# Kernel tuning notes

Hardware: AMD Instinct MI355X
Metric: run time of the kernel (lower is better)

Reference implementation:

```python
import jax, jax.numpy as jnp
import numpy as np

P = 2        # patch size (all 3 dims)
NB = 8       # num_bands
N = 16       # d_state
DTR = 8      # dt_rank = d_model // 16
DCONV = 4    # d_conv
SMAX = 2.0   # smax_dt = smax_B = smax_C


def _ln(x, g, b):
    mu = x.mean(-1, keepdims=True)
    v = ((x - mu) ** 2).mean(-1, keepdims=True)
    return (x - mu) / jnp.sqrt(v + 1e-5) * g + b


def _silu(x):
    return x * jax.nn.sigmoid(x)


def _ssm_layer(x, band, m, rho, Win, bin_, convw, convb, Wx, Wdt, bdt, Alog, Dp,
               Wout, bout, edt, eB, eC, wr, wm):
    # x: [B, L, d_model] -> bidirectional conditioned selective scan (BiFCSSM)
    Bsz, L, _ = x.shape
    ED = convw.shape[0]
    xz = x @ Win + bin_
    xp, z = xz[..., :ED], xz[..., ED:]
    # depthwise causal conv1d over L
    xpad = jnp.pad(xp, ((0, 0), (DCONV - 1, 0), (0, 0)))
    xc = sum(xpad[:, k:k + L, :] * convw[:, k] for k in range(DCONV)) + convb
    xc = _silu(xc)
    dbl = xc @ Wx                                    # [B,L,DTR+2N]
    dt = jax.nn.softplus(dbl[..., :DTR] @ Wdt + bdt)  # [B,L,ED]
    # band/radius/mask conditioned modulation of delta, B, C
    s_dt = SMAX * jax.nn.sigmoid(edt[band][None] + wr[0] * rho[None] + wm[0] * m)
    s_B = SMAX * jax.nn.sigmoid(eB[band][None] + wr[1] * rho[None] + wm[1] * m)
    s_C = SMAX * jax.nn.sigmoid(eC[band][None] + wr[2] * rho[None] + wm[2] * m)
    dt = dt * s_dt[..., None]
    Bm = dbl[..., DTR:DTR + N] * s_B[..., None]       # [B,L,N]
    Cm = dbl[..., DTR + N:] * s_C[..., None]          # [B,L,N]
    A = -jnp.exp(Alog)                                # [ED,N]
    dA = jnp.exp(dt[..., None] * A)                   # [B,L,ED,N]
    dBu = (dA - 1.0) / A * Bm[:, :, None, :] * xc[..., None]   # exact ZOH
    dA_s = jnp.moveaxis(dA, 1, 0)
    dBu_s = jnp.moveaxis(dBu, 1, 0)
    C_s = jnp.moveaxis(Cm, 1, 0)
    h0 = jnp.zeros((Bsz, ED, N), x.dtype)

    def step(h, inp):
        a, bu, c = inp
        h = a * h + bu
        return h, jnp.einsum('ben,bn->be', h, c)

    _, yf = jax.lax.scan(step, h0, (dA_s, dBu_s, C_s))
    _, yb = jax.lax.scan(step, h0, (dA_s, dBu_s, C_s), reverse=True)
    y = jnp.moveaxis(yf + yb, 0, 1) + Dp * xc
    y = y * _silu(z)
    return y @ Wout + bout


def _fwd(kspace_ri, mask, pe_w, pe_b, pu_w, pu_b, ln_g, ln_b, fn_g, fn_b,
         cond_band, cond_rad_w, cond_mask_w, l0_Win, l0_bin, l0_convw, l0_convb,
         l0_Wx, l0_Wdt, l0_bdt, l0_Alog, l0_D, l0_Wout, l0_bout, l0_edt, l0_eB,
         l0_eC, l0_wr, l0_wm):
    Bsz, C, nx, ny, nz = kspace_ri.shape
    gx, gy, gz = nx // P, ny // P, nz // P
    L = gx * gy * gz
    # patch embed (Conv3d, kernel==stride) as blocked einsum
    xr = kspace_ri.reshape(Bsz, C, gx, P, gy, P, gz, P)
    x = jnp.einsum('bcxiyjzk,dcijk->bdxyz', xr, pe_w) + pe_b[None, :, None, None, None]
    DM = x.shape[1]
    x = x.reshape(Bsz, DM, L).transpose(0, 2, 1)               # [B,L,D]
    m = mask.reshape(Bsz, 1, gx, P, gy, P, gz, P).mean(axis=(3, 5, 7)).reshape(Bsz, L)
    m = jnp.clip(m, 0.0, 1.0)
    # raster scan ordering: identity permutation, rho_bar, band ids
    rho = jnp.arange(L, dtype=x.dtype) / float(L - 1)
    band = jnp.clip(jnp.floor(rho * NB).astype(jnp.int32), 0, NB - 1)
    # condition tokens
    cond = cond_band[band][None] + rho[None, :, None] * cond_rad_w + m[:, :, None] * cond_mask_w
    h = _ln(x + cond, ln_g, ln_b)
    h = h + _ssm_layer(_ln(h, fn_g, fn_b), band, m, rho, l0_Win, l0_bin, l0_convw,
                       l0_convb, l0_Wx, l0_Wdt, l0_bdt, l0_Alog, l0_D, l0_Wout,
                       l0_bout, l0_edt, l0_eB, l0_eC, l0_wr, l0_wm)
    # patch unembed (ConvTranspose3d, kernel==stride) as blocked einsum
    hg = h.transpose(0, 2, 1).reshape(Bsz, DM, gx, gy, gz)
    out = jnp.einsum('bdxyz,dcijk->bcxiyjzk', hg, pu_w).reshape(Bsz, C, nx, ny, nz)
    out = out + pu_b[None, :, None, None, None]
    return kspace_ri + out


def setup_inputs() -> dict:
    key = jax.random.key(0)
    ks = jax.random.split(key, 24)
    ED, DM, CIN = 256, 128, 16

    def nrm(k, shape, s):
        return jax.random.normal(k, shape, jnp.float32) * s

    return {
        'kspace_ri': jax.random.normal(ks[0], (1, CIN, 64, 64, 16), jnp.float32),
        'mask': jax.random.uniform(ks[1], (1, 1, 64, 64, 16), jnp.float32),
        'pe_w': nrm(ks[2], (DM, CIN, P, P, P), 0.09),
        'pe_b': nrm(ks[3], (DM,), 0.02),
        'pu_w': nrm(ks[4], (DM, CIN, P, P, P), 0.05),
        'pu_b': jnp.zeros((CIN,), jnp.float32),
        'ln_g': jnp.ones((DM,), jnp.float32),
        'ln_b': jnp.zeros((DM,), jnp.float32),
        'fn_g': jnp.ones((DM,), jnp.float32),
        'fn_b': jnp.zeros((DM,), jnp.float32),
        'cond_band': nrm(ks[5], (NB, DM), 0.02),
        'cond_rad_w': nrm(ks[6], (DM,), 0.02),
        'cond_mask_w': nrm(ks[7], (DM,), 0.02),
        'l0_Win': nrm(ks[8], (DM, 2 * ED), 0.05),
        'l0_bin': jnp.zeros((2 * ED,), jnp.float32),
        'l0_convw': nrm(ks[9], (ED, DCONV), 0.2),
        'l0_convb': jnp.zeros((ED,), jnp.float32),
        'l0_Wx': nrm(ks[10], (ED, DTR + 2 * N), 0.05),
        'l0_Wdt': nrm(ks[11], (DTR, ED), 0.1),
        'l0_bdt': jnp.full((ED,), -3.0, jnp.float32),
        'l0_Alog': jnp.log(jnp.tile(jnp.arange(1, N + 1, dtype=jnp.float32), (ED, 1))),
        'l0_D': jnp.ones((ED,), jnp.float32),
        'l0_Wout': nrm(ks[12], (ED, DM), 0.05),
        'l0_bout': jnp.zeros((DM,), jnp.float32),
        'l0_edt': nrm(ks[13], (NB,), 0.1),
        'l0_eB': nrm(ks[14], (NB,), 0.1),
        'l0_eC': nrm(ks[15], (NB,), 0.1),
        'l0_wr': nrm(ks[16], (3,), 0.1),
        'l0_wm': nrm(ks[17], (3,), 0.1),
    }


def reference(kspace_ri, mask, pe_w, pe_b, pu_w, pu_b, ln_g, ln_b, fn_g, fn_b,
              cond_band, cond_rad_w, cond_mask_w, l0_Win, l0_bin, l0_convw,
              l0_convb, l0_Wx, l0_Wdt, l0_bdt, l0_Alog, l0_D, l0_Wout, l0_bout,
              l0_edt, l0_eB, l0_eC, l0_wr, l0_wm):
    return _fwd(kspace_ri, mask, pe_w, pe_b, pu_w, pu_b, ln_g, ln_b, fn_g, fn_b,
                cond_band, cond_rad_w, cond_mask_w, l0_Win, l0_bin, l0_convw,
                l0_convb, l0_Wx, l0_Wdt, l0_bdt, l0_Alog, l0_D, l0_Wout, l0_bout,
                l0_edt, l0_eB, l0_eC, l0_wr, l0_wm)
```

## Files before the change

### kernel.cpp

```cpp
#include <hip/hip_runtime.h>
#include <hip/hip_bf16.h>

#define L_TOK 8192
#define NCh 512
#define CLh 16
#define NSEG 8
#define CPS (NCh / NSEG)
#define LOG2E 1.44269504088896f

typedef short bf16x8 __attribute__((ext_vector_type(8)));
typedef float f32x4 __attribute__((ext_vector_type(4)));

static __device__ __forceinline__ float nexp2(float x) {
#if __has_builtin(__builtin_amdgcn_exp2f)
    return __builtin_amdgcn_exp2f(x);
#else
    return exp2f(x);
#endif
}
static __device__ __forceinline__ float sigm(float x) {
    return 1.f / (1.f + nexp2(-x * LOG2E));
}
static __device__ __forceinline__ ushort f2bf(float x) {
    union { float f; uint u; } v; v.f = x;
    uint r = v.u + 0x7fffu + ((v.u >> 16) & 1u);
    return (ushort)(r >> 16);
}
static __device__ __forceinline__ float bf2f(ushort h) {
    union { float f; uint u; } v; v.u = ((uint)h) << 16;
    return v.f;
}
static __device__ __forceinline__ void f2hl(float x, ushort* hi, ushort* lo) {
    ushort h = f2bf(x);
    *hi = h;
    *lo = f2bf(x - bf2f(h));
}

#define W_PE   0
#define W_WIN  16384
#define W_WOUT 81920
#define W_PU   114688
#define W_PROJ 131072
#define W_TOT  212992

__global__ __launch_bounds__(256) void prep_k(const float* __restrict__ pe_w, const float* __restrict__ Win,
                                              const float* __restrict__ Wx, const float* __restrict__ Wdt,
                                              const float* __restrict__ Wout, const float* __restrict__ pu_w,
                                              const float* __restrict__ mask,
                                              ushort* __restrict__ wH, ushort* __restrict__ wL,
                                              float* __restrict__ mbuf) {
    int b = blockIdx.x;
    if (b >= 832) {
        int l = (b - 832) * 256 + threadIdx.x;
        int xg = l >> 8, yg = (l >> 3) & 31, zg = l & 7;
        float s = 0.f;
        for (int i2 = 0; i2 < 2; ++i2)
            for (int j2 = 0; j2 < 2; ++j2)
                for (int k2 = 0; k2 < 2; ++k2)
                    s += mask[(2 * xg + i2) * 1024 + (2 * yg + j2) * 16 + 2 * zg + k2];
        s *= 0.125f;
        mbuf[l] = fminf(fmaxf(s, 0.f), 1.f);
        return;
    }
    int i = b * 256 + threadIdx.x;
    float v;
    if (i < 16384) {
        v = pe_w[i];
    } else if (i < 81920) {
        int j = i - 16384; int n = j >> 7, k = j & 127;
        v = Win[k * 512 + n];
    } else if (i < 114688) {
        int j = i - 81920; int n = j >> 8, k = j & 255;
        v = Wout[k * 128 + n];
    } else if (i < 131072) {
        int j = i - 114688; int n = j >> 7, k = j & 127;
        v = pu_w[k * 128 + n];
    } else {
        int j = i - 131072; int n = j >> 8, k = j & 255;
        if (n < 256) {
            float s = 0.f;
#pragma unroll
            for (int r = 0; r < 8; ++r) s += Wx[k * 40 + r] * Wdt[r * 256 + n];
            v = s;
        } else if (n < 288) {
            v = Wx[k * 40 + 8 + (n - 256)];
        } else {
            v = 0.f;
        }
    }
    ushort h, lo; f2hl(v, &h, &lo);
    wH[i] = h; wL[i] = lo;
}

__global__ __launch_bounds__(256) void embed_ln_k(const float* __restrict__ ks,
                                                  const ushort* __restrict__ wH, const ushort* __restrict__ wL,
                                                  const float* __restrict__ pe_b, const float* __restrict__ cond_band,
                                                  const float* __restrict__ cond_rad, const float* __restrict__ cond_mask,
                                                  const float* __restrict__ mbuf,
                                                  const float* __restrict__ ln_g, const float* __restrict__ ln_b,
                                                  const float* __restrict__ fn_g, const float* __restrict__ fn_b,
                                                  float* __restrict__ h_,
                                                  ushort* __restrict__ hnH, ushort* __restrict__ hnL) {
    __shared__ __align__(16) char smem[50176];
    ushort (*AsH)[72] = (ushort(*)[72])(smem);
    ushort (*AsL)[72] = (ushort(*)[72])(smem + 2304);
    ushort (*BsH)[72] = (ushort(*)[72])(smem + 4608);
    ushort (*BsL)[72] = (ushort(*)[72])(smem + 23040);
    float*  ksb       = (float*)(smem + 41472);
    float  (*Cs)[132] = (float(*)[132])(smem);

    const int tid = threadIdx.x;
    const int lane = tid & 63, wn = tid >> 6;
    const int ln = lane & 15, q = lane >> 4;
    const int mb = blockIdx.x * 16;
    const int xg = mb >> 8, yg0 = (mb >> 3) & 31;

    for (int v = tid; v < 512; v += 256) {
        int seg = v >> 2, zq = v & 3;
        int cc = seg >> 3, i2 = (seg >> 2) & 1, yy = seg & 3;
        float4 t4 = *(const float4*)&ks[cc * 65536 + (2 * xg + i2) * 1024 + (2 * yg0 + yy) * 16 + zq * 4];
        int la = seg * 17 + zq * 4;
        ksb[la] = t4.x; ksb[la + 1] = t4.y; ksb[la + 2] = t4.z; ksb[la + 3] = t4.w;
    }

    f32x4 acc[2];
    acc[0] = (f32x4){0.f, 0.f, 0.f, 0.f};
    acc[1] = (f32x4){0.f, 0.f, 0.f, 0.f};

    for (int kc = 0; kc < 128; kc += 64) {
        __syncthreads();
        for (int u = tid; u < 1024; u += 256) {
            int r = u >> 6, kk = u & 63;
            int k = kc + kk;
            int cc = k >> 3, ijk = k & 7;
            int i2 = (ijk >> 2) & 1, j2 = (ijk >> 1) & 1, k2 = ijk & 1;
            int seg = (cc * 2 + i2) * 4 + (r >> 3) * 2 + j2;
            float v = ksb[seg * 17 + (r & 7) * 2 + k2];
            ushort hh, ll; f2hl(v, &hh, &ll);
            AsH[r][kk] = hh; AsL[r][kk] = ll;
        }
        for (int u = tid; u < 1024; u += 256) {
            int n = u >> 3, g = u & 7;
            *(uint4*)&BsH[n][g * 8] = *(const uint4*)&wH[W_PE + n * 128 + kc + g * 8];
            *(uint4*)&BsL[n][g * 8] = *(const uint4*)&wL[W_PE + n * 128 + kc + g * 8];
        }
        __syncthreads();
#pragma unroll
        for (int ks_ = 0; ks_ < 64; ks_ += 32) {
            const int kk = ks_ + q * 8;
            bf16x8 ah = *(const bf16x8*)&AsH[ln][kk];
            bf16x8 al = *(const bf16x8*)&AsL[ln][kk];
#pragma unroll
            for (int cb = 0; cb < 2; ++cb) {
                bf16x8 bh = *(const bf16x8*)&BsH[wn * 32 + cb * 16 + ln][kk];
                bf16x8 bl = *(const bf16x8*)&BsL[wn * 32 + cb * 16 + ln][kk];
                acc[cb] = __builtin_amdgcn_mfma_f32_16x16x32_bf16(ah, bh, acc[cb], 0, 0, 0);
                acc[cb] = __builtin_amdgcn_mfma_f32_16x16x32_bf16(ah, bl, acc[cb], 0, 0, 0);
                acc[cb] = __builtin_amdgcn_mfma_f32_16x16x32_bf16(al, bh, acc[cb], 0, 0, 0);
            }
        }
    }
    __syncthreads();
#pragma unroll
    for (int cb = 0; cb < 2; ++cb) {
#pragma unroll
        for (int r = 0; r < 4; ++r) {
            int row = q * 4 + r;
            int col = wn * 32 + cb * 16 + ln;
            int l = mb + row;
            float rho = (float)l * (1.0f / 8191.0f);
            int band = min(7, (int)(rho * 8.0f));
            Cs[row][col] = acc[cb][r] + pe_b[col] + cond_band[band * 128 + col]
                           + rho * cond_rad[col] + mbuf[l] * cond_mask[col];
        }
    }
    __syncthreads();
    {
        int row = tid >> 4, j = tid & 15;
        int l = mb + row;
        float v8[8];
        float s = 0.f, s2 = 0.f;
#pragma unroll
        for (int i = 0; i < 8; ++i) {
            float v = Cs[row][j * 8 + i];
            v8[i] = v; s += v; s2 += v * v;
        }
#pragma unroll
        for (int o = 1; o < 16; o <<= 1) { s += __shfl_xor(s, o, 16); s2 += __shfl_xor(s2, o, 16); }
        float mu = s * (1.f / 128.f);
        float var = s2 * (1.f / 128.f) - mu * mu;
        float rstd = rsqrtf(fmaxf(var, 0.f) + 1e-5f);
        float hv[8];
        s = 0.f; s2 = 0.f;
#pragma unroll
        for (int i = 0; i < 8; ++i) {
            int col = j * 8 + i;
            float h = (v8[i] - mu) * rstd * ln_g[col] + ln_b[col];
            hv[i] = h; s += h; s2 += h * h;
        }
#pragma unroll
        for (int i = 0; i < 8; i += 4)
            *(float4*)&h_[(size_t)l * 128 + j * 8 + i] = make_float4(hv[i], hv[i + 1], hv[i + 2], hv[i + 3]);
#pragma unroll
        for (int o = 1; o < 16; o <<= 1) { s += __shfl_xor(s, o, 16); s2 += __shfl_xor(s2, o, 16); }
        mu = s * (1.f / 128.f);
        var = s2 * (1.f / 128.f) - mu * mu;
        rstd = rsqrtf(fmaxf(var, 0.f) + 1e-5f);
        union { ushort u[8]; uint4 v4; } oh, ol;
#pragma unroll
        for (int i = 0; i < 8; ++i) {
            int col = j * 8 + i;
            float o2 = (hv[i] - mu) * rstd * fn_g[col] + fn_b[col];
            ushort hh, ll; f2hl(o2, &hh, &ll);
            oh.u[i] = hh; ol.u[i] = ll;
        }
        *(uint4*)&hnH[(size_t)l * 128 + j * 8] = oh.v4;
        *(uint4*)&hnL[(size_t)l * 128 + j * 8] = ol.v4;
    }
}

__global__ __launch_bounds__(256) void win_k(const ushort* __restrict__ Ah, const ushort* __restrict__ Al,
                                             const ushort* __restrict__ wH, const ushort* __restrict__ wL,
                                             const float* __restrict__ bin_,
                                             float* __restrict__ xp, float* __restrict__ sz) {
    __shared__ ushort AsH[64][72], AsL[64][72];
    __shared__ ushort BsH[64][72], BsL[64][72];
    const int tid = threadIdx.x;
    const int lane = tid & 63, wave = tid >> 6;
    const int wm = wave & 1, wn = wave >> 1;
    const int ln = lane & 15, q = lane >> 4;
    const int mb = blockIdx.x * 64, nb = blockIdx.y * 64;

    f32x4 acc[2][2];
#pragma unroll
    for (int rb = 0; rb < 2; ++rb)
#pragma unroll
        for (int cb = 0; cb < 2; ++cb) acc[rb][cb] = (f32x4){0.f, 0.f, 0.f, 0.f};

    for (int kc = 0; kc < 128; kc += 64) {
        __syncthreads();
        for (int u = tid; u < 512; u += 256) {
            int r = u >> 3, g = u & 7;
            size_t go = (size_t)(mb + r) * 128 + kc + g * 8;
            *(uint4*)&AsH[r][g * 8] = *(const uint4*)&Ah[go];
            *(uint4*)&AsL[r][g * 8] = *(const uint4*)&Al[go];
        }
        for (int u = tid; u < 512; u += 256) {
            int n = u >> 3, g = u & 7;
            size_t go = (size_t)(W_WIN) + (size_t)(nb + n) * 128 + kc + g * 8;
            *(uint4*)&BsH[n][g * 8] = *(const uint4*)&wH[go];
            *(uint4*)&BsL[n][g * 8] = *(const uint4*)&wL[go];
        }
        __syncthreads();
#pragma unroll
        for (int ks_ = 0; ks_ < 64; ks_ += 32) {
            const int kk = ks_ + q * 8;
            bf16x8 ah[2], al[2], bh[2], bl[2];
#pragma unroll
            for (int rb = 0; rb < 2; ++rb) {
                ah[rb] = *(const bf16x8*)&AsH[wm * 32 + rb * 16 + ln][kk];
                al[rb] = *(const bf16x8*)&AsL[wm * 32 + rb * 16 + ln][kk];
            }
#pragma unroll
            for (int cb = 0; cb < 2; ++cb) {
                bh[cb] = *(const bf16x8*)&BsH[wn * 32 + cb * 16 + ln][kk];
                bl[cb] = *(const bf16x8*)&BsL[wn * 32 + cb * 16 + ln][kk];
            }
#pragma unroll
            for (int rb = 0; rb < 2; ++rb)
#pragma unroll
                for (int cb = 0; cb < 2; ++cb) {
                    acc[rb][cb] = __builtin_amdgcn_mfma_f32_16x16x32_bf16(ah[rb], bh[cb], acc[rb][cb], 0, 0, 0);
                    acc[rb][cb] = __builtin_amdgcn_mfma_f32_16x16x32_bf16(ah[rb], bl[cb], acc[rb][cb], 0, 0, 0);
                    acc[rb][cb] = __builtin_amdgcn_mfma_f32_16x16x32_bf16(al[rb], bh[cb], acc[rb][cb], 0, 0, 0);
                }
        }
    }
#pragma unroll
    for (int rb = 0; rb < 2; ++rb)
#pragma unroll
        for (int cb = 0; cb < 2; ++cb)
#pragma unroll
            for (int r = 0; r < 4; ++r) {
                int l = mb + wm * 32 + rb * 16 + q * 4 + r;
                int col = nb + wn * 32 + cb * 16 + ln;
                float v = acc[rb][cb][r] + bin_[col];
                if (col < 256) {
                    xp[(size_t)l * 256 + col] = v;
                } else {
                    sz[(size_t)l * 256 + (col - 256)] = v * sigm(v);
                }
            }
}

__global__ __launch_bounds__(512) void proj_k(const float* __restrict__ xp,
                                              const float* __restrict__ convw, const float* __restrict__ convb,
                                              const ushort* __restrict__ wH, const ushort* __restrict__ wL,
                                              const float* __restrict__ bdt, const float* __restrict__ mbuf,
                                              const float* __restrict__ edt, const float* __restrict__ eB,
                                              const float* __restrict__ eC, const float* __restrict__ wr,
                                              const float* __restrict__ wm,
                                              float* __restrict__ xc, float* __restrict__ dt,
                                              float* __restrict__ Bm, float* __restrict__ Cm) {
    __shared__ __align__(16) char smem[52224];
    ushort (*AsH)[264] = (ushort(*)[264])(smem);
    ushort (*AsL)[264] = (ushort(*)[264])(smem + 16896);
    ushort (*BsH)[72]  = (ushort(*)[72])(smem + 33792);
    ushort (*BsL)[72]  = (ushort(*)[72])(smem + 43008);
    const int tid = threadIdx.x;
    const int mb = blockIdx.x * 32;

    {
        const int cg = tid & 63;
        const int rg = tid >> 6;
        const int c0 = cg * 4;
        float4 cb4 = *(const float4*)&convb[c0];
        float4 cw0 = *(const float4*)&convw[(c0 + 0) * 4];
        float4 cw1 = *(const float4*)&convw[(c0 + 1) * 4];
        float4 cw2 = *(const float4*)&convw[(c0 + 2) * 4];
        float4 cw3 = *(const float4*)&convw[(c0 + 3) * 4];
        const int lbase = mb + rg * 4;
        float4 zero = make_float4(0.f, 0.f, 0.f, 0.f);
        float4 x0 = (lbase - 3 >= 0) ? *(const float4*)&xp[(size_t)(lbase - 3) * 256 + c0] : zero;
        float4 x1 = (lbase - 2 >= 0) ? *(const float4*)&xp[(size_t)(lbase - 2) * 256 + c0] : zero;
        float4 x2 = (lbase - 1 >= 0) ? *(const float4*)&xp[(size_t)(lbase - 1) * 256 + c0] : zero;
#pragma unroll
        for (int rr = 0; rr < 4; ++rr) {
            int l = lbase + rr;
            float4 x3 = *(const float4*)&xp[(size_t)l * 256 + c0];
            float o0 = cb4.x + x0.x * cw0.x + x1.x * cw0.y + x2.x * cw0.z + x3.x * cw0.w;
            float o1 = cb4.y + x0.y * cw1.x + x1.y * cw1.y + x2.y * cw1.z + x3.y * cw1.w;
            float o2 = cb4.z + x0.z * cw2.x + x1.z * cw2.y + x2.z * cw2.z + x3.z * cw2.w;
            float o3 = cb4.w + x0.w * cw3.x + x1.w * cw3.y + x2.w * cw3.z + x3.w * cw3.w;
            o0 *= sigm(o0); o1 *= sigm(o1); o2 *= sigm(o2); o3 *= sigm(o3);
            *(float4*)&xc[(size_t)l * 256 + c0] = make_float4(o0, o1, o2, o3);
            union { ushort u[4]; uint2 v2; } hh, ll;
            f2hl(o0, &hh.u[0], &ll.u[0]); f2hl(o1, &hh.u[1], &ll.u[1]);
            f2hl(o2, &hh.u[2], &ll.u[2]); f2hl(o3, &hh.u[3], &ll.u[3]);
            int row = l - mb;
            *(uint2*)&AsH[row][c0] = hh.v2;
            *(uint2*)&AsL[row][c0] = ll.v2;
            x0 = x1; x1 = x2; x2 = x3;
        }
    }
    __syncthreads();

    const int lane = tid & 63, wave = tid >> 6;
    const int wm2 = wave & 1, wn4 = wave >> 1;
    const int ln = lane & 15, q = lane >> 4;
    for (int it = 0; it < 5; ++it) {
        int nb = it * 64;
        f32x4 acc = (f32x4){0.f, 0.f, 0.f, 0.f};
        for (int kc = 0; kc < 256; kc += 64) {
            __syncthreads();
            {
                int u = tid;
                int n = u >> 3, g = u & 7;
                size_t go = (size_t)(W_PROJ) + (size_t)(nb + n) * 256 + kc + g * 8;
                *(uint4*)&BsH[n][g * 8] = *(const uint4*)&wH[go];
                *(uint4*)&BsL[n][g * 8] = *(const uint4*)&wL[go];
            }
            __syncthreads();
#pragma unroll
            for (int ks_ = 0; ks_ < 64; ks_ += 32) {
                const int kka = kc + ks_ + q * 8;
                const int kkb = ks_ + q * 8;
                bf16x8 ah = *(const bf16x8*)&AsH[wm2 * 16 + ln][kka];
                bf16x8 al = *(const bf16x8*)&AsL[wm2 * 16 + ln][kka];
                bf16x8 bh = *(const bf16x8*)&BsH[wn4 * 16 + ln][kkb];
                bf16x8 bl = *(const bf16x8*)&BsL[wn4 * 16 + ln][kkb];
                acc = __builtin_amdgcn_mfma_f32_16x16x32_bf16(ah, bh, acc, 0, 0, 0);
                acc = __builtin_amdgcn_mfma_f32_16x16x32_bf16(ah, bl, acc, 0, 0, 0);
                acc = __builtin_amdgcn_mfma_f32_16x16x32_bf16(al, bh, acc, 0, 0, 0);
            }
        }
#pragma unroll
        for (int r = 0; r < 4; ++r) {
            int l = mb + wm2 * 16 + q * 4 + r;
            int col = nb + wn4 * 16 + ln;
            float v = acc[r];
            float rho = (float)l * (1.0f / 8191.0f);
            int band = min(7, (int)(rho * 8.0f));
            float mv = mbuf[l];
            if (col < 256) {
                float sc0 = 2.0f * sigm(edt[band] + wr[0] * rho + wm[0] * mv);
                float v2 = v + bdt[col];
                float sp = (v2 > 20.f) ? v2 : log1pf(expf(v2));
                dt[(size_t)l * 256 + col] = sp * sc0;
            } else if (col < 272) {
                float sc1 = 2.0f * sigm(eB[band] + wr[1] * rho + wm[1] * mv);
                Bm[(size_t)l * 16 + (col - 256)] = v * sc1;
            } else if (col < 288) {
                float sc2 = 2.0f * sigm(eC[band] + wr[2] * rho + wm[2] * mv);
                Cm[(size_t)l * 16 + (col - 272)] = v * sc2;
            }
        }
    }
}

__global__ __launch_bounds__(256, 4) void scan0_k(const float* __restrict__ dt, const float* __restrict__ xc,
                                                  const float* __restrict__ Bm, const float* __restrict__ Alog,
                                                  float* __restrict__ Hb, float* __restrict__ sdtb) {
    const int c = blockIdx.x, dir = blockIdx.y, e = threadIdx.x;
    __shared__ float bms[CLh][16];
    for (int idx = e; idx < CLh * 16; idx += 256)
        bms[idx >> 4][idx & 15] = Bm[c * (CLh * 16) + idx];
    float A2[16], iv[16], h[16];
#pragma unroll
    for (int n = 0; n < 16; ++n) {
        float ea = nexp2(Alog[e * 16 + n] * LOG2E);
        A2[n] = -ea * LOG2E;
        iv[n] = -1.0f / ea;
        h[n] = 0.f;
    }
    const int base = c * CLh;
    float cu[8], cx[8], nu[8], nx[8];
#pragma unroll
    for (int j = 0; j < 8; ++j) {
        int p = dir ? (CLh - 1 - j) : j;
        cu[j] = dt[(size_t)(base + p) * 256 + e];
        cx[j] = xc[(size_t)(base + p) * 256 + e];
    }
    __syncthreads();
    float sdt = 0.f;
#pragma unroll
    for (int g = 0; g < CLh / 8; ++g) {
        if (g + 1 < CLh / 8) {
#pragma unroll
            for (int j = 0; j < 8; ++j) {
                int s = (g + 1) * 8 + j;
                int p = dir ? (CLh - 1 - s) : s;
                nu[j] = dt[(size_t)(base + p) * 256 + e];
                nx[j] = xc[(size_t)(base + p) * 256 + e];
            }
        }
#pragma unroll
        for (int j = 0; j < 8; ++j) {
            int s = g * 8 + j;
            int p = dir ? (CLh - 1 - s) : s;
            float u = cu[j], xv = cx[j];
            union { float4 v[4]; float f[16]; } bb;
            const float4* bp = (const float4*)&bms[p][0];
            bb.v[0] = bp[0]; bb.v[1] = bp[1]; bb.v[2] = bp[2]; bb.v[3] = bp[3];
#pragma unroll
            for (int n = 0; n < 16; ++n) {
                float a = nexp2(A2[n] * u);
                float w = xv * bb.f[n] * iv[n];
                h[n] = a * (h[n] + w) - w;
            }
            sdt += u;
        }
#pragma unroll
        for (int j = 0; j < 8; ++j) { cu[j] = nu[j]; cx[j] = nx[j]; }
    }
    const size_t hofs = (size_t)(dir * NCh + c) * 4096 + e * 16;
#pragma unroll
    for (int j = 0; j < 4; ++j)
        *(float4*)&Hb[hofs + 4 * j] = make_float4(h[4 * j], h[4 * j + 1], h[4 * j + 2], h[4 * j + 3]);
    if (dir == 0) sdtb[c * 256 + e] = sdt;
}

__global__ __launch_bounds__(256) void combine1_k(const float* __restrict__ Hb, const float* __restrict__ sdtb,
                                                  const float* __restrict__ Alog,
                                                  float* __restrict__ Hpp, float* __restrict__ cumsdtb,
                                                  float* __restrict__ segq, float* __restrict__ segsdt) {
    const int gid = blockIdx.x * 256 + threadIdx.x;
    const int seg = gid >> 13;
    const int r = gid & 8191;
    const int d1 = r >> 12, en = r & 4095, e1 = en >> 4;
    const float A2e = -nexp2(Alog[en] * LOG2E) * LOG2E;
    float hi = 0.f, cum = 0.f;
    for (int k = 0; k < CPS; ++k) {
        const int pos = seg * CPS + k;
        const int c2 = d1 ? (NCh - 1 - pos) : pos;
        const size_t o2 = (size_t)(d1 * NCh + c2) * 4096 + en;
        const float sv = sdtb[c2 * 256 + e1];
        Hpp[o2] = hi;
        if ((en & 15) == 0) cumsdtb[(d1 * NCh + c2) * 256 + e1] = cum;
        hi = nexp2(A2e * sv) * hi + Hb[o2];
        cum += sv;
    }
    segq[(d1 * NSEG + seg) * 4096 + en] = hi;
    if ((en & 15) == 0) segsdt[(d1 * NSEG + seg) * 256 + e1] = cum;
}

__global__ __launch_bounds__(64) void combine2_k(const float* __restrict__ segq, const float* __restrict__ segsdt,
                                                 const float* __restrict__ Alog, float* __restrict__ segpre) {
    const int gid = blockIdx.x * 64 + threadIdx.x;
    const int d1 = gid >> 12, en = gid & 4095, e1 = en >> 4;
    const float A2e = -nexp2(Alog[en] * LOG2E) * LOG2E;
    float hi = 0.f;
#pragma unroll
    for (int s = 0; s < NSEG; ++s) {
        segpre[(d1 * NSEG + s) * 4096 + en] = hi;
        hi = nexp2(A2e * segsdt[(d1 * NSEG + s) * 256 + e1]) * hi + segq[(d1 * NSEG + s) * 4096 + en];
    }
}

template <int DIR>
static __device__ __forceinline__ void scan_dir(const float* __restrict__ dt, const float* __restrict__ xc,
                                                int base, int e,
                                                const float (*bms)[16], const float (*cms)[16],
                                                const float* A2, const float* iv,
                                                float* h, float* yreg) {
    float cu[8], cx[8], nu[8], nx[8];
#pragma unroll
    for (int j = 0; j < 8; ++j) {
        const int p = DIR ? (CLh - 1 - j) : j;
        cu[j] = dt[(size_t)(base + p) * 256 + e];
        cx[j] = xc[(size_t)(base + p) * 256 + e];
    }
#pragma unroll
    for (int g = 0; g < CLh / 8; ++g) {
        if (g + 1 < CLh / 8) {
#pragma unroll
            for (int j = 0; j < 8; ++j) {
                const int s = (g + 1) * 8 + j;
                const int p = DIR ? (CLh - 1 - s) : s;
                nu[j] = dt[(size_t)(base + p) * 256 + e];
                nx[j] = xc[(size_t)(base + p) * 256 + e];
            }
        }
#pragma unroll
        for (int j = 0; j < 8; ++j) {
            const int s = g * 8 + j;
            const int p = DIR ? (CLh - 1 - s) : s;
            float u = cu[j], xv = cx[j];
            union { float4 v[4]; float f[16]; } bb, cc;
            const float4* bp = (const float4*)&bms[p][0];
            bb.v[0] = bp[0]; bb.v[1] = bp[1]; bb.v[2] = bp[2]; bb.v[3] = bp[3];
            const float4* cp = (const float4*)&cms[p][0];
            cc.v[0] = cp[0]; cc.v[1] = cp[1]; cc.v[2] = cp[2]; cc.v[3] = cp[3];
            float y = 0.f;
#pragma unroll
            for (int n = 0; n < 16; ++n) {
                float a = nexp2(A2[n] * u);
                float w = xv * bb.f[n] * iv[n];
                h[n] = a * (h[n] + w) - w;
                y += h[n] * cc.f[n];
            }
            yreg[p] = y;
        }
#pragma unroll
        for (int j = 0; j < 8; ++j) { cu[j] = nu[j]; cx[j] = nx[j]; }
    }
}

__global__ __launch_bounds__(512) void scan1g_k(const float* __restrict__ dt, const float* __restrict__ xc,
                                                const float* __restrict__ Bm, const float* __restrict__ Cm,
                                                const float* __restrict__ Alog,
                                                const float* __restrict__ Hpp, const float* __restrict__ cumsdtb,
                                                const float* __restrict__ segpre,
                                                const float* __restrict__ sz, const float* __restrict__ Dp,
                                                ushort* __restrict__ AHo, ushort* __restrict__ ALo) {
    const int c = blockIdx.x;
    const int tid = threadIdx.x;
    const int dir = tid >> 8;
    const int e = tid & 255;
    __shared__ float bms[CLh][16];
    __shared__ float cms[CLh][16];
    __shared__ float ysum[CLh][256];
    for (int idx = tid; idx < CLh * 16; idx += 512) {
        bms[idx >> 4][idx & 15] = Bm[c * (CLh * 16) + idx];
        cms[idx >> 4][idx & 15] = Cm[c * (CLh * 16) + idx];
    }
    float A2[16], iv[16], h[16];
#pragma unroll
    for (int n = 0; n < 16; ++n) {
        float ea = nexp2(Alog[e * 16 + n] * LOG2E);
        A2[n] = -ea * LOG2E;
        iv[n] = -1.0f / ea;
    }
    {
        const int pos = dir ? (NCh - 1 - c) : c;
        const int seg = pos / CPS;
        const float cum = cumsdtb[(dir * NCh + c) * 256 + e];
        const size_t hofs = (size_t)(dir * NCh + c) * 4096 + e * 16;
        const size_t so = (size_t)(dir * NSEG + seg) * 4096 + e * 16;
#pragma unroll
        for (int jj = 0; jj < 4; ++jj) {
            float4 hv = *(const float4*)&Hpp[hofs + 4 * jj];
            float4 sv = *(const float4*)&segpre[so + 4 * jj];
            h[4 * jj + 0] = hv.x + nexp2(A2[4 * jj + 0] * cum) * sv.x;
            h[4 * jj + 1] = hv.y + nexp2(A2[4 * jj + 1] * cum) * sv.y;
            h[4 * jj + 2] = hv.z + nexp2(A2[4 * jj + 2] * cum) * sv.z;
            h[4 * jj + 3] = hv.w + nexp2(A2[4 * jj + 3] * cum) * sv.w;
        }
    }
    const int base = c * CLh;
    float yreg[CLh];
    __syncthreads();
    if (dir == 0) {
        scan_dir<0>(dt, xc, base, e, bms, cms, A2, iv, h, yreg);
    } else {
        scan_dir<1>(dt, xc, base, e, bms, cms, A2, iv, h, yreg);
    }
    __syncthreads();
    if (dir == 0) {
#pragma unroll
        for (int l = 0; l < CLh; ++l) ysum[l][e] = yreg[l];
    }
    __syncthreads();
    if (dir == 1) {
        float dpv = Dp[e];
#pragma unroll
        for (int l = 0; l < CLh; ++l) {
            size_t gl = (size_t)(base + l) * 256 + e;
            float a = (ysum[l][e] + yreg[l] + dpv * xc[gl]) * sz[gl];
            ushort hh, ll; f2hl(a, &hh, &ll);
            AHo[gl] = hh; ALo[gl] = ll;
        }
    }
}

__global__ __launch_bounds__(512) void wu_k(const ushort* __restrict__ AH, const ushort* __restrict__ AL,
                                            const ushort* __restrict__ wH, const ushort* __restrict__ wL,
                                            const float* __restrict__ bout, const float* __restrict__ h_,
                                            const float* __restrict__ pu_b, const float* __restrict__ ks,
                                            float* __restrict__ out) {
    __shared__ __align__(16) char smem[70656];
    ushort (*AsH)[264] = (ushort(*)[264])(smem);
    ushort (*AsL)[264] = (ushort(*)[264])(smem + 16896);
    ushort (*BsH)[72]  = (ushort(*)[72])(smem + 33792);
    ushort (*BsL)[72]  = (ushort(*)[72])(smem + 52224);
    ushort (*hfH)[136] = (ushort(*)[136])(smem);
    ushort (*hfL)[136] = (ushort(*)[136])(smem + 8704);

    const int tid = threadIdx.x;
    const int lane = tid & 63, wave = tid >> 6;
    const int wm = wave & 1, wn = wave >> 1;
    const int ln = lane & 15, q = lane >> 4;
    const int mb = blockIdx.x * 32;

    for (int u = tid; u < 1024; u += 512) {
        int r = u >> 5, g = u & 31;
        size_t go = (size_t)(mb + r) * 256 + g * 8;
        *(uint4*)&AsH[r][g * 8] = *(const uint4*)&AH[go];
        *(uint4*)&AsL[r][g * 8] = *(const uint4*)&AL[go];
    }

    f32x4 acc[2];
    acc[0] = (f32x4){0.f, 0.f, 0.f, 0.f};
    acc[1] = (f32x4){0.f, 0.f, 0.f, 0.f};

    for (int kc = 0; kc < 256; kc += 64) {
        __syncthreads();
        for (int u = tid; u < 1024; u += 512) {
            int n = u >> 3, g = u & 7;
            size_t go = (size_t)(W_WOUT) + (size_t)n * 256 + kc + g * 8;
            *(uint4*)&BsH[n][g * 8] = *(const uint4*)&wH[go];
            *(uint4*)&BsL[n][g * 8] = *(const uint4*)&wL[go];
        }
        __syncthreads();
#pragma unroll
        for (int ks_ = 0; ks_ < 64; ks_ += 32) {
            const int kka = kc + ks_ + q * 8;
            const int kkb = ks_ + q * 8;
            bf16x8 ah = *(const bf16x8*)&AsH[wm * 16 + ln][kka];
            bf16x8 al = *(const bf16x8*)&AsL[wm * 16 + ln][kka];
#pragma unroll
            for (int cb = 0; cb < 2; ++cb) {
                bf16x8 bh = *(const bf16x8*)&BsH[wn * 32 + cb * 16 + ln][kkb];
                bf16x8 bl = *(const bf16x8*)&BsL[wn * 32 + cb * 16 + ln][kkb];
                acc[cb] = __builtin_amdgcn_mfma_f32_16x16x32_bf16(ah, bh, acc[cb], 0, 0, 0);
                acc[cb] = __builtin_amdgcn_mfma_f32_16x16x32_bf16(ah, bl, acc[cb], 0, 0, 0);
                acc[cb] = __builtin_amdgcn_mfma_f32_16x16x32_bf16(al, bh, acc[cb], 0, 0, 0);
            }
        }
    }
    __syncthreads();
#pragma unroll
    for (int cb = 0; cb < 2; ++cb)
#pragma unroll
        for (int r = 0; r < 4; ++r) {
            int row = wm * 16 + q * 4 + r;
            int col = wn * 32 + cb * 16 + ln;
            float v = acc[cb][r] + bout[col] + h_[(size_t)(mb + row) * 128 + col];
            ushort hh, ll; f2hl(v, &hh, &ll);
            hfH[row][col] = hh;
            hfL[row][col] = ll;
        }
    __syncthreads();

    f32x4 acc2[2];
    acc2[0] = (f32x4){0.f, 0.f, 0.f, 0.f};
    acc2[1] = (f32x4){0.f, 0.f, 0.f, 0.f};
    for (int kc = 0; kc < 128; kc += 64) {
        __syncthreads();
        for (int u = tid; u < 1024; u += 512) {
            int n = u >> 3, g = u & 7;
            size_t go = (size_t)(W_PU) + (size_t)n * 128 + kc + g * 8;
            *(uint4*)&BsH[n][g * 8] = *(const uint4*)&wH[go];
            *(uint4*)&BsL[n][g * 8] = *(const uint4*)&wL[go];
        }
        __syncthreads();
#pragma unroll
        for (int ks_ = 0; ks_ < 64; ks_ += 32) {
            const int kka = kc + ks_ + q * 8;
            const int kkb = ks_ + q * 8;
            bf16x8 ah = *(const bf16x8*)&hfH[wm * 16 + ln][kka];
            bf16x8 al = *(const bf16x8*)&hfL[wm * 16 + ln][kka];
#pragma unroll
            for (int cb = 0; cb < 2; ++cb) {
                bf16x8 bh = *(const bf16x8*)&BsH[wn * 32 + cb * 16 + ln][kkb];
                bf16x8 bl = *(const bf16x8*)&BsL[wn * 32 + cb * 16 + ln][kkb];
                acc2[cb] = __builtin_amdgcn_mfma_f32_16x16x32_bf16(ah, bh, acc2[cb], 0, 0, 0);
                acc2[cb] = __builtin_amdgcn_mfma_f32_16x16x32_bf16(ah, bl, acc2[cb], 0, 0, 0);
                acc2[cb] = __builtin_amdgcn_mfma_f32_16x16x32_bf16(al, bh, acc2[cb], 0, 0, 0);
            }
        }
    }
#pragma unroll
    for (int cb = 0; cb < 2; ++cb)
#pragma unroll
        for (int r = 0; r < 4; ++r) {
            int l = mb + wm * 16 + q * 4 + r;
            int col = wn * 32 + cb * 16 + ln;
            int xg = l >> 8, yg = (l >> 3) & 31, zg = l & 7;
            int cch = col >> 3, ijk = col & 7;
            int i2 = (ijk >> 2) & 1, j2 = (ijk >> 1) & 1, k2 = ijk & 1;
            size_t idx = (size_t)((cch * 64 + 2 * xg + i2) * 64 + (2 * yg + j2)) * 16 + 2 * zg + k2;
            out[idx] = acc2[cb][r] + pu_b[cch] + ks[idx];
        }
}

extern "C" void kernel_launch(void* const* d_in, const int* in_sizes, int n_in,
                              void* d_out, int out_size, void* d_ws, size_t ws_size,
                              hipStream_t stream) {
    const float* ks    = (const float*)d_in[0];
    const float* mask  = (const float*)d_in[1];
    const float* pe_w  = (const float*)d_in[2];
    const float* pe_b  = (const float*)d_in[3];
    const float* pu_w  = (const float*)d_in[4];
    const float* pu_b  = (const float*)d_in[5];
    const float* ln_g  = (const float*)d_in[6];
    const float* ln_b  = (const float*)d_in[7];
    const float* fn_g  = (const float*)d_in[8];
    const float* fn_b  = (const float*)d_in[9];
    const float* cond_band = (const float*)d_in[10];
    const float* cond_rad  = (const float*)d_in[11];
    const float* cond_mask = (const float*)d_in[12];
    const float* Win   = (const float*)d_in[13];
    const float* bin_  = (const float*)d_in[14];
    const float* convw = (const float*)d_in[15];
    const float* convb = (const float*)d_in[16];
    const float* Wx    = (const float*)d_in[17];
    const float* Wdt   = (const float*)d_in[18];
    const float* bdt   = (const float*)d_in[19];
    const float* Alog  = (const float*)d_in[20];
    const float* Dp    = (const float*)d_in[21];
    const float* Wout  = (const float*)d_in[22];
    const float* bout  = (const float*)d_in[23];
    const float* edt   = (const float*)d_in[24];
    const float* eB    = (const float*)d_in[25];
    const float* eC    = (const float*)d_in[26];
    const float* wr    = (const float*)d_in[27];
    const float* wm    = (const float*)d_in[28];
    float* out = (float*)d_out;

    char* base = (char*)d_ws;
    size_t o = 0;
    auto alloc = [&](size_t bytes) { char* p = base + o; o += (bytes + 255) & ~(size_t)255; return p; };
    float*  mbuf = (float*)alloc(32768);
    ushort* wH   = (ushort*)alloc(W_TOT * 2);
    ushort* wL   = (ushort*)alloc(W_TOT * 2);
    float*  h_   = (float*)alloc(4194304);
    ushort* hnH  = (ushort*)alloc(2097152);
    ushort* hnL  = (ushort*)alloc(2097152);
    float*  xp   = (float*)alloc(8388608);
    float*  sz   = (float*)alloc(8388608);
    float*  xc   = (float*)alloc(8388608);
    float*  dt   = (float*)alloc(8388608);
    float*  Bm   = (float*)alloc(524288);
    float*  Cm   = (float*)alloc(524288);
    float*  Hb   = (float*)alloc((size_t)2 * NCh * 4096 * 4);
    float*  Hpp  = (float*)alloc((size_t)2 * NCh * 4096 * 4);
    float*  sdtb = (float*)alloc((size_t)NCh * 256 * 4);
    float*  cumsdtb = (float*)alloc((size_t)2 * NCh * 256 * 4);
    float*  segq    = (float*)alloc((size_t)2 * NSEG * 4096 * 4);
    float*  segsdt  = (float*)alloc((size_t)2 * NSEG * 256 * 4);
    float*  segpre  = (float*)alloc((size_t)2 * NSEG * 4096 * 4);
    ushort* AHo  = (ushort*)alloc(4194304);
    ushort* ALo  = (ushort*)alloc(4194304);

    prep_k<<<864, 256, 0, stream>>>(pe_w, Win, Wx, Wdt, Wout, pu_w, mask, wH, wL, mbuf);
    embed_ln_k<<<512, 256, 0, stream>>>(ks, wH, wL, pe_b, cond_band, cond_rad, cond_mask, mbuf,
                                        ln_g, ln_b, fn_g, fn_b, h_, hnH, hnL);
    win_k<<<dim3(128, 8), 256, 0, stream>>>(hnH, hnL, wH, wL, bin_, xp, sz);
    proj_k<<<256, 512, 0, stream>>>(xp, convw, convb, wH, wL, bdt, mbuf, edt, eB, eC, wr, wm,
                                    xc, dt, Bm, Cm);
    scan0_k<<<dim3(NCh, 2), 256, 0, stream>>>(dt, xc, Bm, Alog, Hb, sdtb);
    combine1_k<<<256, 256, 0, stream>>>(Hb, sdtb, Alog, Hpp, cumsdtb, segq, segsdt);
    combine2_k<<<128, 64, 0, stream>>>(segq, segsdt, Alog, segpre);
    scan1g_k<<<NCh, 512, 0, stream>>>(dt, xc, Bm, Cm, Alog, Hpp, cumsdtb, segpre, sz, Dp, AHo, ALo);
    wu_k<<<256, 512, 0, stream>>>(AHo, ALo, wH, wL, bout, h_, pu_b, ks, out);
}
```

Measured before the change: 249.0 us.

## Fuse weight prep into embed kernel, prefetch proj weights, merge scan directions

The weight-conversion kernel is folded into the embed/LN launch as extra blocks. The embed blocks now convert pe_w and pool the mask locally, so they no longer depend on prep output. proj_k register-prefetches the next weight tile before the barrier, scan0 runs both directions in one 512-thread block, and scan1g splits the output epilogue across both directions using register-held xc, which removes a barrier and global reloads. Together these cut one launch and some memory latency, at the cost of redundant conversion work and more register pressure.

```diff
diff --git a/kernel.cpp b/kernel.cpp
--- a/kernel.cpp
+++ b/kernel.cpp
@@ -43,65 +43,68 @@
 #define W_PROJ 131072
 #define W_TOT  212992
 
-__global__ __launch_bounds__(256) void prep_k(const float* __restrict__ pe_w, const float* __restrict__ Win,
-                                              const float* __restrict__ Wx, const float* __restrict__ Wdt,
-                                              const float* __restrict__ Wout, const float* __restrict__ pu_w,
-                                              const float* __restrict__ mask,
-                                              ushort* __restrict__ wH, ushort* __restrict__ wL,
-                                              float* __restrict__ mbuf) {
-    int b = blockIdx.x;
-    if (b >= 832) {
-        int l = (b - 832) * 256 + threadIdx.x;
-        int xg = l >> 8, yg = (l >> 3) & 31, zg = l & 7;
-        float s = 0.f;
-        for (int i2 = 0; i2 < 2; ++i2)
-            for (int j2 = 0; j2 < 2; ++j2)
-                for (int k2 = 0; k2 < 2; ++k2)
-                    s += mask[(2 * xg + i2) * 1024 + (2 * yg + j2) * 16 + 2 * zg + k2];
-        s *= 0.125f;
-        mbuf[l] = fminf(fmaxf(s, 0.f), 1.f);
-        return;
-    }
-    int i = b * 256 + threadIdx.x;
-    float v;
-    if (i < 16384) {
-        v = pe_w[i];
-    } else if (i < 81920) {
-        int j = i - 16384; int n = j >> 7, k = j & 127;
-        v = Win[k * 512 + n];
-    } else if (i < 114688) {
-        int j = i - 81920; int n = j >> 8, k = j & 255;
-        v = Wout[k * 128 + n];
-    } else if (i < 131072) {
-        int j = i - 114688; int n = j >> 7, k = j & 127;
-        v = pu_w[k * 128 + n];
-    } else {
-        int j = i - 131072; int n = j >> 8, k = j & 255;
-        if (n < 256) {
-            float s = 0.f;
-#pragma unroll
-            for (int r = 0; r < 8; ++r) s += Wx[k * 40 + r] * Wdt[r * 256 + n];
-            v = s;
-        } else if (n < 288) {
-            v = Wx[k * 40 + 8 + (n - 256)];
-        } else {
-            v = 0.f;
-        }
-    }
-    ushort h, lo; f2hl(v, &h, &lo);
-    wH[i] = h; wL[i] = lo;
-}
-
 __global__ __launch_bounds__(256) void embed_ln_k(const float* __restrict__ ks,
-                                                  const ushort* __restrict__ wH, const ushort* __restrict__ wL,
+                                                  const float* __restrict__ pe_w,
+                                                  const float* __restrict__ Win,
+                                                  const float* __restrict__ Wx, const float* __restrict__ Wdt,
+                                                  const float* __restrict__ Wout, const float* __restrict__ pu_w,
+                                                  const float* __restrict__ mask,
                                                   const float* __restrict__ pe_b, const float* __restrict__ cond_band,
                                                   const float* __restrict__ cond_rad, const float* __restrict__ cond_mask,
-                                                  const float* __restrict__ mbuf,
                                                   const float* __restrict__ ln_g, const float* __restrict__ ln_b,
                                                   const float* __restrict__ fn_g, const float* __restrict__ fn_b,
+                                                  ushort* __restrict__ wH, ushort* __restrict__ wL,
+                                                  float* __restrict__ mbuf,
                                                   float* __restrict__ h_,
                                                   ushort* __restrict__ hnH, ushort* __restrict__ hnL) {
+    const int tid = threadIdx.x;
+    if (blockIdx.x >= 512) {
+        int b = blockIdx.x - 512;
+        if (b >= 832) {
+            int l = (b - 832) * 256 + tid;
+            int xg = l >> 8, yg = (l >> 3) & 31, zg = l & 7;
+            float s = 0.f;
+            for (int i2 = 0; i2 < 2; ++i2)
+                for (int j2 = 0; j2 < 2; ++j2)
+                    for (int k2 = 0; k2 < 2; ++k2)
+                        s += mask[(2 * xg + i2) * 1024 + (2 * yg + j2) * 16 + 2 * zg + k2];
+            s *= 0.125f;
+            mbuf[l] = fminf(fmaxf(s, 0.f), 1.f);
+            return;
+        }
+        int i = b * 256 + tid;
+        float v;
+        if (i < 16384) {
+            v = pe_w[i];
+        } else if (i < 81920) {
+            int j = i - 16384; int n = j >> 7, k = j & 127;
+            v = Win[k * 512 + n];
+        } else if (i < 114688) {
+            int j = i - 81920; int n = j >> 8, k = j & 255;
+            v = Wout[k * 128 + n];
+        } else if (i < 131072) {
+            int j = i - 114688; int n = j >> 7, k = j & 127;
+            v = pu_w[k * 128 + n];
+        } else {
+            int j = i - 131072; int n = j >> 8, k = j & 255;
+            if (n < 256) {
+                float s = 0.f;
+#pragma unroll
+                for (int r = 0; r < 8; ++r) s += Wx[k * 40 + r] * Wdt[r * 256 + n];
+                v = s;
+            } else if (n < 288) {
+                v = Wx[k * 40 + 8 + (n - 256)];
+            } else {
+                v = 0.f;
+            }
+        }
+        ushort h, lo; f2hl(v, &h, &lo);
+        wH[i] = h; wL[i] = lo;
+        return;
+    }
+
     __shared__ __align__(16) char smem[50176];
+    __shared__ float mpool[16];
     ushort (*AsH)[72] = (ushort(*)[72])(smem);
     ushort (*AsL)[72] = (ushort(*)[72])(smem + 2304);
     ushort (*BsH)[72] = (ushort(*)[72])(smem + 4608);
@@ -109,7 +112,6 @@
     float*  ksb       = (float*)(smem + 41472);
     float  (*Cs)[132] = (float(*)[132])(smem);
 
-    const int tid = threadIdx.x;
     const int lane = tid & 63, wn = tid >> 6;
     const int ln = lane & 15, q = lane >> 4;
     const int mb = blockIdx.x * 16;
@@ -121,6 +123,16 @@
         float4 t4 = *(const float4*)&ks[cc * 65536 + (2 * xg + i2) * 1024 + (2 * yg0 + yy) * 16 + zq * 4];
         int la = seg * 17 + zq * 4;
         ksb[la] = t4.x; ksb[la + 1] = t4.y; ksb[la + 2] = t4.z; ksb[la + 3] = t4.w;
+    }
+    if (tid < 16) {
+        int l = mb + tid;
+        int xg2 = l >> 8, yg2 = (l >> 3) & 31, zg2 = l & 7;
+        float s = 0.f;
+        for (int i2 = 0; i2 < 2; ++i2)
+            for (int j2 = 0; j2 < 2; ++j2)
+                for (int k2 = 0; k2 < 2; ++k2)
+                    s += mask[(2 * xg2 + i2) * 1024 + (2 * yg2 + j2) * 16 + 2 * zg2 + k2];
+        mpool[tid] = fminf(fmaxf(s * 0.125f, 0.f), 1.f);
     }
 
     f32x4 acc[2];
@@ -141,8 +153,16 @@
         }
         for (int u = tid; u < 1024; u += 256) {
             int n = u >> 3, g = u & 7;
-            *(uint4*)&BsH[n][g * 8] = *(const uint4*)&wH[W_PE + n * 128 + kc + g * 8];
-            *(uint4*)&BsL[n][g * 8] = *(const uint4*)&wL[W_PE + n * 128 + kc + g * 8];
+            const float* pw = &pe_w[n * 128 + kc + g * 8];
+            float4 p0 = *(const float4*)pw;
+            float4 p1 = *(const float4*)(pw + 4);
+            union { ushort us[8]; uint4 v4; } hh, ll;
+            f2hl(p0.x, &hh.us[0], &ll.us[0]); f2hl(p0.y, &hh.us[1], &ll.us[1]);
+            f2hl(p0.z, &hh.us[2], &ll.us[2]); f2hl(p0.w, &hh.us[3], &ll.us[3]);
+            f2hl(p1.x, &hh.us[4], &ll.us[4]); f2hl(p1.y, &hh.us[5], &ll.us[5]);
+            f2hl(p1.z, &hh.us[6], &ll.us[6]); f2hl(p1.w, &hh.us[7], &ll.us[7]);
+            *(uint4*)&BsH[n][g * 8] = hh.v4;
+            *(uint4*)&BsL[n][g * 8] = ll.v4;
         }
         __syncthreads();
 #pragma unroll
@@ -171,7 +191,7 @@
             float rho = (float)l * (1.0f / 8191.0f);
             int band = min(7, (int)(rho * 8.0f));
             Cs[row][col] = acc[cb][r] + pe_b[col] + cond_band[band * 128 + col]
-                           + rho * cond_rad[col] + mbuf[l] * cond_mask[col];
+                           + rho * cond_rad[col] + mpool[row] * cond_mask[col];
         }
     }
     __syncthreads();
@@ -343,6 +363,9 @@
             x0 = x1; x1 = x2; x2 = x3;
         }
     }
+    const int pn = tid >> 3, pg = tid & 7;
+    uint4 regH = *(const uint4*)&wH[(size_t)W_PROJ + (size_t)pn * 256 + pg * 8];
+    uint4 regL = *(const uint4*)&wL[(size_t)W_PROJ + (size_t)pn * 256 + pg * 8];
     __syncthreads();
 
     const int lane = tid & 63, wave = tid >> 6;
@@ -351,14 +374,18 @@
     for (int it = 0; it < 5; ++it) {
         int nb = it * 64;
         f32x4 acc = (f32x4){0.f, 0.f, 0.f, 0.f};
-        for (int kc = 0; kc < 256; kc += 64) {
+        for (int kci = 0; kci < 4; ++kci) {
+            int kc = kci * 64;
             __syncthreads();
-            {
-                int u = tid;
-                int n = u >> 3, g = u & 7;
-                size_t go = (size_t)(W_PROJ) + (size_t)(nb + n) * 256 + kc + g * 8;
-                *(uint4*)&BsH[n][g * 8] = *(const uint4*)&wH[go];
-                *(uint4*)&BsL[n][g * 8] = *(const uint4*)&wL[go];
+            *(uint4*)&BsH[pn][pg * 8] = regH;
+            *(uint4*)&BsL[pn][pg * 8] = regL;
+            int s = it * 4 + kci;
+            if (s < 19) {
+                int s2 = s + 1;
+                int nb2 = (s2 >> 2) * 64, kc2 = (s2 & 3) * 64;
+                size_t go = (size_t)W_PROJ + (size_t)(nb2 + pn) * 256 + kc2 + pg * 8;
+                regH = *(const uint4*)&wH[go];
+                regL = *(const uint4*)&wL[go];
             }
             __syncthreads();
 #pragma unroll
@@ -398,12 +425,14 @@
     }
 }
 
-__global__ __launch_bounds__(256, 4) void scan0_k(const float* __restrict__ dt, const float* __restrict__ xc,
-                                                  const float* __restrict__ Bm, const float* __restrict__ Alog,
-                                                  float* __restrict__ Hb, float* __restrict__ sdtb) {
-    const int c = blockIdx.x, dir = blockIdx.y, e = threadIdx.x;
+__global__ __launch_bounds__(512) void scan0_k(const float* __restrict__ dt, const float* __restrict__ xc,
+                                               const float* __restrict__ Bm, const float* __restrict__ Alog,
+                                               float* __restrict__ Hb, float* __restrict__ sdtb) {
+    const int c = blockIdx.x;
+    const int tid = threadIdx.x;
+    const int dir = tid >> 8, e = tid & 255;
     __shared__ float bms[CLh][16];
-    for (int idx = e; idx < CLh * 16; idx += 256)
+    for (int idx = tid; idx < CLh * 16; idx += 512)
         bms[idx >> 4][idx & 15] = Bm[c * (CLh * 16) + idx];
     float A2[16], iv[16], h[16];
 #pragma unroll
@@ -436,9 +465,9 @@
         }
 #pragma unroll
         for (int j = 0; j < 8; ++j) {
+            float u = cu[j], xv = cx[j];
             int s = g * 8 + j;
             int p = dir ? (CLh - 1 - s) : s;
-            float u = cu[j], xv = cx[j];
             union { float4 v[4]; float f[16]; } bb;
             const float4* bp = (const float4*)&bms[p][0];
             bb.v[0] = bp[0]; bb.v[1] = bp[1]; bb.v[2] = bp[2]; bb.v[3] = bp[3];
@@ -502,7 +531,7 @@
                                                 int base, int e,
                                                 const float (*bms)[16], const float (*cms)[16],
                                                 const float* A2, const float* iv,
-                                                float* h, float* yreg) {
+                                                float* h, float* yreg, float* cxl) {
     float cu[8], cx[8], nu[8], nx[8];
 #pragma unroll
     for (int j = 0; j < 8; ++j) {
@@ -544,6 +573,8 @@
 #pragma unroll
         for (int j = 0; j < 8; ++j) { cu[j] = nu[j]; cx[j] = nx[j]; }
     }
+#pragma unroll
+    for (int j = 0; j < 8; ++j) cxl[j] = cx[j];
 }
 
 __global__ __launch_bounds__(512) void scan1g_k(const float* __restrict__ dt, const float* __restrict__ xc,
@@ -559,7 +590,8 @@
     const int e = tid & 255;
     __shared__ float bms[CLh][16];
     __shared__ float cms[CLh][16];
-    __shared__ float ysum[CLh][256];
+    __shared__ float ysF[8][256];
+    __shared__ float ysB[8][256];
     for (int idx = tid; idx < CLh * 16; idx += 512) {
         bms[idx >> 4][idx & 15] = Bm[c * (CLh * 16) + idx];
         cms[idx >> 4][idx & 15] = Cm[c * (CLh * 16) + idx];
@@ -588,25 +620,34 @@
         }
     }
     const int base = c * CLh;
-    float yreg[CLh];
+    float yreg[CLh], cxl[8];
     __syncthreads();
     if (dir == 0) {
-        scan_dir<0>(dt, xc, base, e, bms, cms, A2, iv, h, yreg);
+        scan_dir<0>(dt, xc, base, e, bms, cms, A2, iv, h, yreg, cxl);
+#pragma unroll
+        for (int j = 0; j < 8; ++j) ysF[j][e] = yreg[j];
     } else {
-        scan_dir<1>(dt, xc, base, e, bms, cms, A2, iv, h, yreg);
+        scan_dir<1>(dt, xc, base, e, bms, cms, A2, iv, h, yreg, cxl);
+#pragma unroll
+        for (int j = 0; j < 8; ++j) ysB[j][e] = yreg[8 + j];
     }
     __syncthreads();
+    const float dpv = Dp[e];
     if (dir == 0) {
 #pragma unroll
-        for (int l = 0; l < CLh; ++l) ysum[l][e] = yreg[l];
-    }
-    __syncthreads();
-    if (dir == 1) {
-        float dpv = Dp[e];
-#pragma unroll
-        for (int l = 0; l < CLh; ++l) {
+        for (int j = 0; j < 8; ++j) {
+            const int l = 8 + j;
             size_t gl = (size_t)(base + l) * 256 + e;
-            float a = (ysum[l][e] + yreg[l] + dpv * xc[gl]) * sz[gl];
+            float a = (yreg[l] + ysB[j][e] + dpv * cxl[j]) * sz[gl];
+            ushort hh, ll; f2hl(a, &hh, &ll);
+            AHo[gl] = hh; ALo[gl] = ll;
+        }
+    } else {
+#pragma unroll
+        for (int j = 0; j < 8; ++j) {
+            const int l = 7 - j;
+            size_t gl = (size_t)(base + l) * 256 + e;
+            float a = (ysF[l][e] + yreg[l] + dpv * cxl[j]) * sz[gl];
             ushort hh, ll; f2hl(a, &hh, &ll);
             AHo[gl] = hh; ALo[gl] = ll;
         }
@@ -783,13 +824,14 @@
     ushort* AHo  = (ushort*)alloc(4194304);
     ushort* ALo  = (ushort*)alloc(4194304);
 
-    prep_k<<<864, 256, 0, stream>>>(pe_w, Win, Wx, Wdt, Wout, pu_w, mask, wH, wL, mbuf);
-    embed_ln_k<<<512, 256, 0, stream>>>(ks, wH, wL, pe_b, cond_band, cond_rad, cond_mask, mbuf,
-                                        ln_g, ln_b, fn_g, fn_b, h_, hnH, hnL);
+    embed_ln_k<<<1376, 256, 0, stream>>>(ks, pe_w, Win, Wx, Wdt, Wout, pu_w, mask,
+                                         pe_b, cond_band, cond_rad, cond_mask,
+                                         ln_g, ln_b, fn_g, fn_b,
+                                         wH, wL, mbuf, h_, hnH, hnL);
     win_k<<<dim3(128, 8), 256, 0, stream>>>(hnH, hnL, wH, wL, bin_, xp, sz);
     proj_k<<<256, 512, 0, stream>>>(xp, convw, convb, wH, wL, bdt, mbuf, edt, eB, eC, wr, wm,
                                     xc, dt, Bm, Cm);
-    scan0_k<<<dim3(NCh, 2), 256, 0, stream>>>(dt, xc, Bm, Alog, Hb, sdtb);
+    scan0_k<<<NCh, 512, 0, stream>>>(dt, xc, Bm, Alog, Hb, sdtb);
     combine1_k<<<256, 256, 0, stream>>>(Hb, sdtb, Alog, Hpp, cumsdtb, segq, segsdt);
     combine2_k<<<128, 64, 0, stream>>>(segq, segsdt, Alog, segpre);
     scan1g_k<<<NCh, 512, 0, stream>>>(dt, xc, Bm, Cm, Alog, Hpp, cumsdtb, segpre, sz, Dp, AHo, ALo);
```

After: 272.6 us (median of 2 runs). +9.5%, slower.
